# Performance work log

Hardware: AMD Instinct MI355X
Metric: run time of the kernel (lower is better)

## Reference

```python
import jax, jax.numpy as jnp
import numpy as np

SKIP = 91
PREEMPH = 0.85
N = 33554432  # 2**25 samples


def setup_inputs() -> dict:
    key = jax.random.key(0)
    sig = jax.random.normal(key, (N,), dtype=jnp.float32) * 0.1
    return {"sig": sig}


def _preemph_scan(y, coef):
    # First-order IIR: out[0] = y[0]; out[i] = y[i] + coef * out[i-1]
    # Expressed as an associative scan over pairs (a, b) representing x -> a*x + b.
    a = jnp.full_like(y, coef)

    def combine(e1, e2):
        a1, b1 = e1
        a2, b2 = e2
        return a1 * a2, b2 + a2 * b1

    _, out = jax.lax.associative_scan(combine, (a, y))
    return out


def reference(sig):
    y = _preemph_scan(sig, jnp.float32(PREEMPH))
    # drop first `skip` samples, zero-pad the tail (same length)
    y = jnp.concatenate([y[SKIP:], jnp.zeros((SKIP,), dtype=y.dtype)])
    out = jnp.clip(32768.0 * y, -32768.0, 32767.0).astype(jnp.int16)
    return out
```

## Files before the change

kernel.cpp:

```cpp
#include <hip/hip_runtime.h>


#define BLOCK   256
#define SKIP    91
#define COEF    0.85f
#define CHUNK_N 256
#define CHUNKS  8
#define SEG     (CHUNKS * CHUNK_N)
#define WPB     (BLOCK / 64)
#define TILE    (WPB * SEG)

typedef int v4i __attribute__((ext_vector_type(4)));

__device__ __forceinline__ int cvt16(float v) {
    float s = v * 32768.f;
    s = fminf(fmaxf(s, -32768.f), 32767.f);
    return (int)s;
}

__device__ __forceinline__ float4 ld_guard(const float* __restrict__ sig,
                                           long yb, long n) {
    float4 x;
    x.x = (yb + 0 >= 0 && yb + 0 < n) ? sig[yb + 0] : 0.f;
    x.y = (yb + 1 >= 0 && yb + 1 < n) ? sig[yb + 1] : 0.f;
    x.z = (yb + 2 >= 0 && yb + 2 < n) ? sig[yb + 2] : 0.f;
    x.w = (yb + 3 >= 0 && yb + 3 < n) ? sig[yb + 3] : 0.f;
    return x;
}

template <bool FAST>
__device__ __forceinline__ void run_seg(const float* __restrict__ sig,
                                        int* __restrict__ out,
                                        long segBase, long ln, int lane) {
    const float K1  = COEF * COEF * COEF * COEF;
    const float K2  = K1 * K1;
    const float K4  = K2 * K2;
    const float K8  = K4 * K4;
    const float K16 = K8 * K8;
    const float C1 = COEF, C2 = COEF * COEF, C3 = C2 * COEF;
    const float wpow = exp2f((float)(lane + 1) * (4.0f * -0.23446525109f));

    float s0, s1, s2, s3;
    auto wscan = [&](const float4& x) -> float {
        s0 = x.x;
        s1 = fmaf(s0, COEF, x.y);
        s2 = fmaf(s1, COEF, x.z);
        s3 = fmaf(s2, COEF, x.w);
        float t = s3, u;
        u = __shfl_up(t, 1, 64);  t = (lane >= 1)  ? fmaf(u, K1,  t) : t;
        u = __shfl_up(t, 2, 64);  t = (lane >= 2)  ? fmaf(u, K2,  t) : t;
        u = __shfl_up(t, 4, 64);  t = (lane >= 4)  ? fmaf(u, K4,  t) : t;
        u = __shfl_up(t, 8, 64);  t = (lane >= 8)  ? fmaf(u, K8,  t) : t;
        u = __shfl_up(t, 16, 64); t = (lane >= 16) ? fmaf(u, K16, t) : t;
        return t;
    };

    float4 xw, xs[CHUNKS];
    if constexpr (FAST) {
        const float* base = sig + segBase + 4 * (long)lane;
        xw = *reinterpret_cast<const float4*>(base - 164);
#pragma unroll
        for (int c = 0; c < CHUNKS; ++c)
            xs[c] = *reinterpret_cast<const float4*>(base + (SKIP + 1) + c * CHUNK_N);
        __builtin_amdgcn_sched_barrier(0);
    } else {
        xw = ld_guard(sig, segBase - 164 + 4 * (long)lane, ln);
#pragma unroll
        for (int c = 0; c < CHUNKS; ++c)
            xs[c] = ld_guard(sig, segBase + (SKIP + 1) + (long)c * CHUNK_N
                                  + 4 * (long)lane, ln);
    }

    float tw   = wscan(xw);
    float y_in = __shfl(tw, 63, 64);

    const long oLim = ln - SKIP;

#pragma unroll
    for (int c = 0; c < CHUNKS; ++c) {
        const long o0 = segBase + (long)c * CHUNK_N;

        float t = wscan(xs[c]);
        float L = fmaf(wpow, y_in, t);
        float p = __shfl_up(L, 1, 64);
        if (lane == 0) p = y_in;

        v4i iv;
        iv.x = cvt16(p);
        iv.y = cvt16(fmaf(p, C1, s0));
        iv.z = cvt16(fmaf(p, C2, s1));
        iv.w = cvt16(fmaf(p, C3, s2));

        y_in = __shfl(L, 63, 64);

        const long ob = o0 + 4 * (long)lane;
        if constexpr (FAST) {
            *reinterpret_cast<v4i*>(out + ob) = iv;
        } else {
            if (ob + 0 >= oLim) iv.x = 0;
            if (ob + 1 >= oLim) iv.y = 0;
            if (ob + 2 >= oLim) iv.z = 0;
            if (ob + 3 >= oLim) iv.w = 0;
            if (ob + 0 < ln) out[ob + 0] = iv.x;
            if (ob + 1 < ln) out[ob + 1] = iv.y;
            if (ob + 2 < ln) out[ob + 2] = iv.z;
            if (ob + 3 < ln) out[ob + 3] = iv.w;
        }
    }
}

__global__ __launch_bounds__(BLOCK, 6) void preemph_kernel(
        const float* __restrict__ sig, int* __restrict__ out, int n) {
    const long ln   = n;
    const int  lane = threadIdx.x & 63;
    const long segBase = (long)blockIdx.x * TILE + (long)(threadIdx.x >> 6) * SEG;
    if (segBase >= ln) return;

    const bool fast = (segBase >= 164) && (segBase + SEG + SKIP + 1 <= ln);
    if (fast) run_seg<true >(sig, out, segBase, ln, lane);
    else      run_seg<false>(sig, out, segBase, ln, lane);
}

extern "C" void kernel_launch(void* const* d_in, const int* in_sizes, int n_in,
                              void* d_out, int out_size, void* d_ws, size_t ws_size,
                              hipStream_t stream) {
    const float* sig = (const float*)d_in[0];
    int* out = (int*)d_out;
    int n = in_sizes[0];
    int grid = (int)(((long)n + TILE - 1) / TILE);
    preemph_kernel<<<grid, BLOCK, 0, stream>>>(sig, out, n);
}
```

Baseline: 230.2 us.

## Scan all chunks independently and drop serial carry between chunks

Instead of scanning each 256-sample chunk serially and carrying the last value from one chunk into the next, the kernel now runs the wave-level scans of all nine vectors (eight chunks plus the warm-up window) in an interleaved pass. Each chunk's incoming state is approximated by the tail of the previous chunk's local scan alone, since the decay makes older contributions negligible. This removes the serial shuffle dependency chain between chunks and exposes instruction-level parallelism across shuffles. The cost is higher register pressure and a changed numerical approximation of the carry, which could differ slightly in the int16 output.

```diff
diff --git a/kernel.cpp b/kernel.cpp
--- a/kernel.cpp
+++ b/kernel.cpp
@@ -37,63 +37,64 @@
     const float K4  = K2 * K2;
     const float K8  = K4 * K4;
     const float K16 = K8 * K8;
+    const float KS[5] = {K1, K2, K4, K8, K16};
     const float C1 = COEF, C2 = COEF * COEF, C3 = C2 * COEF;
-    const float wpow = exp2f((float)(lane + 1) * (4.0f * -0.23446525109f));
+    const float wq = exp2f((float)lane * (4.0f * -0.23446525109f));
 
-    float s0, s1, s2, s3;
-    auto wscan = [&](const float4& x) -> float {
-        s0 = x.x;
-        s1 = fmaf(s0, COEF, x.y);
-        s2 = fmaf(s1, COEF, x.z);
-        s3 = fmaf(s2, COEF, x.w);
-        float t = s3, u;
-        u = __shfl_up(t, 1, 64);  t = (lane >= 1)  ? fmaf(u, K1,  t) : t;
-        u = __shfl_up(t, 2, 64);  t = (lane >= 2)  ? fmaf(u, K2,  t) : t;
-        u = __shfl_up(t, 4, 64);  t = (lane >= 4)  ? fmaf(u, K4,  t) : t;
-        u = __shfl_up(t, 8, 64);  t = (lane >= 8)  ? fmaf(u, K8,  t) : t;
-        u = __shfl_up(t, 16, 64); t = (lane >= 16) ? fmaf(u, K16, t) : t;
-        return t;
-    };
-
-    float4 xw, xs[CHUNKS];
+    float4 x[9];
     if constexpr (FAST) {
         const float* base = sig + segBase + 4 * (long)lane;
-        xw = *reinterpret_cast<const float4*>(base - 164);
 #pragma unroll
-        for (int c = 0; c < CHUNKS; ++c)
-            xs[c] = *reinterpret_cast<const float4*>(base + (SKIP + 1) + c * CHUNK_N);
-        __builtin_amdgcn_sched_barrier(0);
+        for (int c = 0; c < 8; ++c)
+            x[c] = *reinterpret_cast<const float4*>(base + (SKIP + 1) + c * CHUNK_N);
+        x[8] = *reinterpret_cast<const float4*>(base - 164);
     } else {
-        xw = ld_guard(sig, segBase - 164 + 4 * (long)lane, ln);
 #pragma unroll
-        for (int c = 0; c < CHUNKS; ++c)
-            xs[c] = ld_guard(sig, segBase + (SKIP + 1) + (long)c * CHUNK_N
-                                  + 4 * (long)lane, ln);
+        for (int c = 0; c < 8; ++c)
+            x[c] = ld_guard(sig, segBase + (SKIP + 1) + (long)c * CHUNK_N
+                                 + 4 * (long)lane, ln);
+        x[8] = ld_guard(sig, segBase - 164 + 4 * (long)lane, ln);
     }
 
-    float tw   = wscan(xw);
-    float y_in = __shfl(tw, 63, 64);
+    float t[9], s0[8], s1[8], s2[8];
+#pragma unroll
+    for (int c = 0; c < 9; ++c) {
+        float a0 = x[c].x;
+        float a1 = fmaf(a0, COEF, x[c].y);
+        float a2 = fmaf(a1, COEF, x[c].z);
+        float a3 = fmaf(a2, COEF, x[c].w);
+        if (c < 8) { s0[c] = a0; s1[c] = a1; s2[c] = a2; }
+        t[c] = a3;
+    }
+
+#pragma unroll
+    for (int d = 0; d < 5; ++d) {
+        const int sh = 1 << d;
+        float u[9];
+#pragma unroll
+        for (int c = 0; c < 9; ++c) u[c] = __shfl_up(t[c], sh, 64);
+#pragma unroll
+        for (int c = 0; c < 9; ++c)
+            t[c] = (lane >= sh) ? fmaf(u[c], KS[d], t[c]) : t[c];
+    }
+
+    float tsh[8], Tp[8];
+#pragma unroll
+    for (int c = 0; c < 8; ++c) tsh[c] = __shfl_up(t[c], 1, 64);
+#pragma unroll
+    for (int c = 0; c < 8; ++c) Tp[c] = __shfl(t[c == 0 ? 8 : c - 1], 63, 64);
 
     const long oLim = ln - SKIP;
-
 #pragma unroll
-    for (int c = 0; c < CHUNKS; ++c) {
-        const long o0 = segBase + (long)c * CHUNK_N;
-
-        float t = wscan(xs[c]);
-        float L = fmaf(wpow, y_in, t);
-        float p = __shfl_up(L, 1, 64);
-        if (lane == 0) p = y_in;
-
+    for (int c = 0; c < 8; ++c) {
+        float u = (lane == 0) ? 0.f : tsh[c];
+        float p = fmaf(Tp[c], wq, u);
         v4i iv;
         iv.x = cvt16(p);
-        iv.y = cvt16(fmaf(p, C1, s0));
-        iv.z = cvt16(fmaf(p, C2, s1));
-        iv.w = cvt16(fmaf(p, C3, s2));
-
-        y_in = __shfl(L, 63, 64);
-
-        const long ob = o0 + 4 * (long)lane;
+        iv.y = cvt16(fmaf(p, C1, s0[c]));
+        iv.z = cvt16(fmaf(p, C2, s1[c]));
+        iv.w = cvt16(fmaf(p, C3, s2[c]));
+        const long ob = segBase + (long)c * CHUNK_N + 4 * (long)lane;
         if constexpr (FAST) {
             *reinterpret_cast<v4i*>(out + ob) = iv;
         } else {
```

New measurement: 231.6 us. About the same (+0.6%).
